# Kernel optimization log

Hardware: AMD Instinct MI355X
Metric: run time of the kernel (lower is better)

The kernel has to match this reference:

```python
import jax, jax.numpy as jnp
import numpy as np

EMBED_DIM = 1024
NUM_HEADS = 16
HEAD_DIM = EMBED_DIM // NUM_HEADS


def setup_inputs() -> dict:
    key = jax.random.key(0)
    ks = jax.random.split(key, 5)
    B, S, E = 2, 2048, EMBED_DIM
    # xavier-uniform-ish scale for square linear weights
    lim = float(np.sqrt(6.0 / (E + E)))
    x = jax.random.normal(ks[0], (B, S, E), dtype=jnp.float32)
    Wq = jax.random.uniform(ks[1], (E, E), jnp.float32, -lim, lim)
    Wk = jax.random.uniform(ks[2], (E, E), jnp.float32, -lim, lim)
    Wv = jax.random.uniform(ks[3], (E, E), jnp.float32, -lim, lim)
    Wo = jax.random.uniform(ks[4], (E, E), jnp.float32, -lim, lim)
    z = jnp.zeros((E,), jnp.float32)
    return {"x": x, "Wq": Wq, "bq": z, "Wk": Wk, "bk": z,
            "Wv": Wv, "bv": z, "Wo": Wo, "bo": z}


def reference(x, Wq, bq, Wk, bk, Wv, bv, Wo, bo):
    B, S, E = x.shape
    H, Dh = NUM_HEADS, HEAD_DIM
    # Linear projections (torch Linear: y = x @ W.T + b)
    q = (x @ Wq.T + bq).reshape(B, S, H, Dh).transpose(0, 2, 1, 3)  # [B,H,S,Dh]
    k = (x @ Wk.T + bk).reshape(B, S, H, Dh).transpose(0, 2, 1, 3)
    v = (x @ Wv.T + bv).reshape(B, S, H, Dh).transpose(0, 2, 1, 3)
    # NOTE: module scales by 1/head_dim (not 1/sqrt(head_dim)) — faithful.
    logits = jnp.einsum('bhqd,bhkd->bhqk', q, k) / Dh  # [B,H,S,S]
    attn = jax.nn.softmax(logits, axis=-1)
    vals = jnp.einsum('bhqk,bhkd->bhqd', attn, v)      # [B,H,S,Dh]
    vals = vals.transpose(0, 2, 1, 3).reshape(B, S, E)
    out = vals @ Wo.T + bo
    return out
```

## Files before the change

kernel.cpp:

```cpp
#include <hip/hip_runtime.h>
#include <hip/hip_bf16.h>

#define EDIM 1024
#define NH   16
#define DH   64
#define BB   2
#define SS   2048
#define MM   (BB*SS)

typedef unsigned short u16;
typedef unsigned int   u32;
typedef __attribute__((ext_vector_type(4)))  float f32x4;
typedef __attribute__((ext_vector_type(16))) float f32x16;
typedef __attribute__((ext_vector_type(8)))  short s16x8;

__device__ __forceinline__ u16 f2bf(float x) {
    __hip_bfloat16 b = __float2bfloat16(x);
    return *(u16*)&b;
}
__device__ __forceinline__ u32 cvtpk(float lo, float hi_) {
    u32 r;
    asm("v_cvt_pk_bf16_f32 %0, %1, %2" : "=v"(r) : "v"(lo), "v"(hi_));
    return r;
}
__device__ __forceinline__ void swap32(u32& a, u32& b) {
    asm("v_permlane32_swap_b32 %0, %1" : "+v"(a), "+v"(b));
}

__device__ __forceinline__ void gload16(const void* g, void* l) {
    __builtin_amdgcn_global_load_lds(
        (const __attribute__((address_space(1))) unsigned int*)g,
        (__attribute__((address_space(3))) unsigned int*)l, 16, 0, 0);
}

__global__ __launch_bounds__(256) void convert_all(const float* __restrict__ x,
                                                   const float* __restrict__ Wq,
                                                   const float* __restrict__ Wk,
                                                   const float* __restrict__ Wv,
                                                   const float* __restrict__ Wo,
                                                   u16* __restrict__ xh,
                                                   u16* __restrict__ wqkv,
                                                   u16* __restrict__ woh)
{
    const int i = blockIdx.x * 256 + threadIdx.x;
    const float* src; ushort4* dst; int off;
    if (i < 1048576)      { src = x;  dst = (ushort4*)xh;   off = i; }
    else if (i < 1310720) { src = Wq; dst = (ushort4*)wqkv; off = i - 1048576; }
    else if (i < 1572864) { src = Wk; dst = (ushort4*)wqkv; off = i - 1310720 + 262144; }
    else if (i < 1835008) { src = Wv; dst = (ushort4*)wqkv; off = i - 1572864 + 524288; }
    else                  { src = Wo; dst = (ushort4*)woh;  off = i - 1835008; }
    const int so = (i < 1048576) ? i
                 : (i < 1310720) ? (i - 1048576)
                 : (i < 1572864) ? (i - 1310720)
                 : (i < 1835008) ? (i - 1572864) : (i - 1835008);
    const float4 v = ((const float4*)src)[so];
    ushort4 h;
    h.x = f2bf(v.x); h.y = f2bf(v.y); h.z = f2bf(v.z); h.w = f2bf(v.w);
    dst[off] = h;
}

__global__ __launch_bounds__(256) void gemm_qkv(const u16* __restrict__ A,
                                                const u16* __restrict__ B,
                                                const float* __restrict__ bq,
                                                const float* __restrict__ bk,
                                                const float* __restrict__ bv,
                                                u16* __restrict__ qb,
                                                u16* __restrict__ kb,
                                                u16* __restrict__ vT)
{
    __shared__ __align__(16) u16 As[2][128][64];
    __shared__ __align__(16) u16 Bs[2][128][64];

    const int tid  = threadIdx.x;
    const int lane = tid & 63, wid = tid >> 6;
    const int wm = wid >> 1, wn = wid & 1;
    const int swz = (blockIdx.x & 7) * 96 + (blockIdx.x >> 3);
    const int m0 = (swz & 31) * 128;
    const int n0 = (swz >> 5) * 128;

    const char* Abase = (const char*)(A + (size_t)m0 * 1024);
    const char* Bbase = (const char*)(B + (size_t)n0 * 1024);

    f32x4 acc[4][4];
    #pragma unroll
    for (int i = 0; i < 4; ++i)
        #pragma unroll
        for (int j = 0; j < 4; ++j) acc[i][j] = f32x4{0.f, 0.f, 0.f, 0.f};

    auto stage = [&](int buf, int k0) {
        #pragma unroll
        for (int i = 0; i < 4; ++i) {
            const int flat = i * 256 + tid;
            const int row = flat >> 3, u = flat & 7;
            const size_t so = (size_t)row * 2048 + (size_t)k0 * 2 + ((u ^ (row & 7)) << 4);
            gload16(Abase + so, (char*)As + buf * 16384 + (i * 256 + wid * 64) * 16);
        }
        #pragma unroll
        for (int i = 0; i < 4; ++i) {
            const int flat = i * 256 + tid;
            const int row = flat >> 3, u = flat & 7;
            const size_t so = (size_t)row * 2048 + (size_t)k0 * 2 + ((u ^ (row & 7)) << 4);
            gload16(Bbase + so, (char*)Bs + buf * 16384 + (i * 256 + wid * 64) * 16);
        }
    };
    auto compute = [&](int buf) {
        const char* Ab = (const char*)As + buf * 16384;
        const char* Bb = (const char*)Bs + buf * 16384;
        #pragma unroll
        for (int kk = 0; kk < 2; ++kk) {
            s16x8 af[4], bfr[4];
            #pragma unroll
            for (int i = 0; i < 4; ++i) {
                const int rowA = wm * 64 + i * 16 + (lane & 15);
                af[i] = *(const s16x8*)(Ab + rowA * 128 + (((kk * 4 + (lane >> 4)) ^ (rowA & 7)) << 4));
                const int rowB = wn * 64 + i * 16 + (lane & 15);
                bfr[i] = *(const s16x8*)(Bb + rowB * 128 + (((kk * 4 + (lane >> 4)) ^ (rowB & 7)) << 4));
            }
            #pragma unroll
            for (int i = 0; i < 4; ++i)
                #pragma unroll
                for (int j = 0; j < 4; ++j)
                    acc[i][j] = __builtin_amdgcn_mfma_f32_16x16x32_bf16(af[i], bfr[j], acc[i][j], 0, 0, 0);
        }
    };

    stage(0, 0);
    __syncthreads();
    #pragma unroll 1
    for (int t = 0; t < 15; ++t) {
        stage((t & 1) ^ 1, (t + 1) * 64);
        compute(t & 1);
        __syncthreads();
    }
    compute(1);

    if (n0 < 1024) {
        #pragma unroll
        for (int i = 0; i < 4; ++i) {
            const int mbase = m0 + wm * 64 + i * 16 + ((lane >> 4) * 4);
            #pragma unroll
            for (int j = 0; j < 4; ++j) {
                const int n = n0 + wn * 64 + j * 16 + (lane & 15);
                const float bias = bq[n];
                const int h_ = n >> 6, d_ = n & 63;
                #pragma unroll
                for (int r = 0; r < 4; ++r) {
                    const int m = mbase + r;
                    const int b_ = m >> 11, s_ = m & 2047;
                    qb[((size_t)(b_ * NH + h_) * SS + s_) * DH + d_] = f2bf(acc[i][j][r] + bias);
                }
            }
        }
    } else if (n0 < 2048) {
        #pragma unroll
        for (int i = 0; i < 4; ++i) {
            const int mbase = m0 + wm * 64 + i * 16 + ((lane >> 4) * 4);
            #pragma unroll
            for (int j = 0; j < 4; ++j) {
                const int n = n0 + wn * 64 + j * 16 + (lane & 15);
                const float bias = bk[n - 1024];
                const int h_ = (n >> 6) & 15, d_ = n & 63;
                #pragma unroll
                for (int r = 0; r < 4; ++r) {
                    const int m = mbase + r;
                    const int b_ = m >> 11, s_ = m & 2047;
                    kb[((size_t)(b_ * NH + h_) * SS + s_) * DH + d_] = f2bf(acc[i][j][r] + bias);
                }
            }
        }
    } else {
        #pragma unroll
        for (int i = 0; i < 4; ++i) {
            const int mbase = m0 + wm * 64 + i * 16 + ((lane >> 4) * 4);
            #pragma unroll
            for (int j = 0; j < 4; ++j) {
                const int n = n0 + wn * 64 + j * 16 + (lane & 15);
                const float bias = bv[n - 2048];
                const int hd = n - 2048;
                #pragma unroll
                for (int r = 0; r < 4; ++r) {
                    const int m = mbase + r;
                    const int b_ = m >> 11, s_ = m & 2047;
                    vT[((size_t)(b_ * EDIM) + hd) * SS + s_] = f2bf(acc[i][j][r] + bias);
                }
            }
        }
    }
}

__global__ __launch_bounds__(256) void gemm_out(const u16* __restrict__ A,
                                                const u16* __restrict__ B,
                                                const float* __restrict__ bo,
                                                float* __restrict__ out)
{
    __shared__ __align__(16) u16 As[2][64][64];
    __shared__ __align__(16) u16 Bs[2][128][64];

    const int tid  = threadIdx.x;
    const int lane = tid & 63, wid = tid >> 6;
    const int wm = wid >> 1, wn = wid & 1;
    const int swz = (blockIdx.x & 7) * 64 + (blockIdx.x >> 3);
    const int m0 = (swz & 63) * 64;
    const int n0 = (swz >> 6) * 128;

    const char* Abase = (const char*)(A + (size_t)m0 * 1024);
    const char* Bbase = (const char*)(B + (size_t)n0 * 1024);

    f32x4 acc[2][4];
    #pragma unroll
    for (int i = 0; i < 2; ++i)
        #pragma unroll
        for (int j = 0; j < 4; ++j) acc[i][j] = f32x4{0.f, 0.f, 0.f, 0.f};

    auto stage = [&](int buf, int k0) {
        #pragma unroll
        for (int i = 0; i < 2; ++i) {
            const int flat = i * 256 + tid;
            const int row = flat >> 3, u = flat & 7;
            const size_t so = (size_t)row * 2048 + (size_t)k0 * 2 + ((u ^ (row & 7)) << 4);
            gload16(Abase + so, (char*)As + buf * 8192 + (i * 256 + wid * 64) * 16);
        }
        #pragma unroll
        for (int i = 0; i < 4; ++i) {
            const int flat = i * 256 + tid;
            const int row = flat >> 3, u = flat & 7;
            const size_t so = (size_t)row * 2048 + (size_t)k0 * 2 + ((u ^ (row & 7)) << 4);
            gload16(Bbase + so, (char*)Bs + buf * 16384 + (i * 256 + wid * 64) * 16);
        }
    };
    auto compute = [&](int buf) {
        const char* Ab = (const char*)As + buf * 8192;
        const char* Bb = (const char*)Bs + buf * 16384;
        #pragma unroll
        for (int kk = 0; kk < 2; ++kk) {
            s16x8 af[2], bfr[4];
            #pragma unroll
            for (int i = 0; i < 2; ++i) {
                const int rowA = wm * 32 + i * 16 + (lane & 15);
                af[i] = *(const s16x8*)(Ab + rowA * 128 + (((kk * 4 + (lane >> 4)) ^ (rowA & 7)) << 4));
            }
            #pragma unroll
            for (int j = 0; j < 4; ++j) {
                const int rowB = wn * 64 + j * 16 + (lane & 15);
                bfr[j] = *(const s16x8*)(Bb + rowB * 128 + (((kk * 4 + (lane >> 4)) ^ (rowB & 7)) << 4));
            }
            #pragma unroll
            for (int i = 0; i < 2; ++i)
                #pragma unroll
                for (int j = 0; j < 4; ++j)
                    acc[i][j] = __builtin_amdgcn_mfma_f32_16x16x32_bf16(af[i], bfr[j], acc[i][j], 0, 0, 0);
        }
    };

    stage(0, 0);
    __syncthreads();
    #pragma unroll 1
    for (int t = 0; t < 15; ++t) {
        stage((t & 1) ^ 1, (t + 1) * 64);
        compute(t & 1);
        __syncthreads();
    }
    compute(1);

    #pragma unroll
    for (int i = 0; i < 2; ++i) {
        const int mbase = m0 + wm * 32 + i * 16 + ((lane >> 4) * 4);
        #pragma unroll
        for (int j = 0; j < 4; ++j) {
            const int n = n0 + wn * 64 + j * 16 + (lane & 15);
            #pragma unroll
            for (int r = 0; r < 4; ++r)
                out[(size_t)(mbase + r) * EDIM + n] = acc[i][j][r] + bo[n];
        }
    }
}

__global__ __launch_bounds__(256) void attn_mfma(const u16* __restrict__ q,
                                                 const u16* __restrict__ k,
                                                 const u16* __restrict__ vT,
                                                 u16* __restrict__ valsh)
{
    __shared__ __align__(16) u16 kt[2][128][64];
    __shared__ __align__(16) u16 vt[2][64][128];

    const int tid = threadIdx.x, lane = tid & 63, wid = tid >> 6;
    const int lq = lane & 31, hi = lane >> 5;
    const int swz = (blockIdx.x & 7) * 64 + (blockIdx.x >> 3);
    const int bh = swz >> 4, qt = swz & 15;
    const int b = bh >> 4, h = bh & 15;

    const u16* qg = q + ((size_t)bh * SS + qt * 128 + wid * 32 + lq) * DH + hi * 8;
    s16x8 qf[4];
    #pragma unroll
    for (int ks = 0; ks < 4; ++ks) qf[ks] = *(const s16x8*)(qg + ks * 16);

    f32x16 acc_o[2];
    #pragma unroll
    for (int db = 0; db < 2; ++db)
        #pragma unroll
        for (int r = 0; r < 16; ++r) acc_o[db][r] = 0.f;
    float rs = 0.f;

    const char* kbh = (const char*)(k + (size_t)bh * SS * DH);
    const char* vbh = (const char*)(vT + ((size_t)b * EDIM + h * DH) * SS);

    auto stage = [&](int buf, int c0) {
        #pragma unroll
        for (int i = 0; i < 4; ++i) {
            const int flat = i * 256 + tid;
            const int row = flat >> 3, u = flat & 7;
            gload16(kbh + (size_t)(c0 + row) * 128 + ((u ^ (row & 7)) << 4),
                    (char*)kt + buf * 16384 + (i * 256 + wid * 64) * 16);
        }
        #pragma unroll
        for (int i = 0; i < 4; ++i) {
            const int flat = i * 256 + tid;
            const int row = flat >> 4, u = flat & 15;
            gload16(vbh + (size_t)row * (SS * 2) + (size_t)c0 * 2 + ((u ^ (row & 15)) << 4),
                    (char*)vt + buf * 16384 + (i * 256 + wid * 64) * 16);
        }
    };

    stage(0, 0);
    __syncthreads();

    int buf = 0;
    #pragma unroll 1
    for (int c = 0; c < 16; ++c) {
        if (c < 15) stage(buf ^ 1, (c + 1) * 128);
        const char* ktb = (const char*)kt + buf * 16384;
        const char* vtb = (const char*)vt + buf * 16384;

        #pragma unroll
        for (int kb = 0; kb < 4; ++kb) {
            f32x16 sc;
            #pragma unroll
            for (int r = 0; r < 16; ++r) sc[r] = 0.f;
            const int krow = kb * 32 + lq;
            __builtin_amdgcn_s_setprio(1);
            #pragma unroll
            for (int ks = 0; ks < 4; ++ks) {
                const int u = (ks * 2 + hi) ^ (krow & 7);
                const s16x8 kf = *(const s16x8*)(ktb + krow * 128 + u * 16);
                sc = __builtin_amdgcn_mfma_f32_32x32x16_bf16(kf, qf[ks], sc, 0, 0, 0);
            }
            __builtin_amdgcn_s_setprio(0);

            #pragma unroll
            for (int r = 0; r < 16; ++r) {
                sc[r] = __builtin_amdgcn_exp2f(sc[r] * 0.0225421209f);
                rs += sc[r];
            }

            u32 w0 = cvtpk(sc[0],  sc[1]),  w1 = cvtpk(sc[2],  sc[3]);
            u32 w2 = cvtpk(sc[4],  sc[5]),  w3 = cvtpk(sc[6],  sc[7]);
            u32 w4 = cvtpk(sc[8],  sc[9]),  w5 = cvtpk(sc[10], sc[11]);
            u32 w6 = cvtpk(sc[12], sc[13]), w7 = cvtpk(sc[14], sc[15]);
            swap32(w0, w2);
            swap32(w1, w3);
            swap32(w4, w6);
            swap32(w5, w7);
            union { u32 w[4]; s16x8 v; } pa0, pa1;
            pa0.w[0] = w0; pa0.w[1] = w1; pa0.w[2] = w2; pa0.w[3] = w3;
            pa1.w[0] = w4; pa1.w[1] = w5; pa1.w[2] = w6; pa1.w[3] = w7;

            __builtin_amdgcn_s_setprio(1);
            #pragma unroll
            for (int t = 0; t < 2; ++t) {
                const s16x8 pat = t ? pa1.v : pa0.v;
                const int kst = kb * 2 + t;
                #pragma unroll
                for (int db = 0; db < 2; ++db) {
                    const int vrow = db * 32 + lq;
                    const int u = (kst * 2 + hi) ^ (vrow & 15);
                    const s16x8 vf = *(const s16x8*)(vtb + vrow * 256 + u * 16);
                    acc_o[db] = __builtin_amdgcn_mfma_f32_32x32x16_bf16(pat, vf, acc_o[db], 0, 0, 0);
                }
            }
            __builtin_amdgcn_s_setprio(0);
        }
        __syncthreads();
        buf ^= 1;
    }

    const float rsf = rs + __shfl_xor(rs, 32, 64);
    const float inv = 1.f / rsf;
    float iv[16];
    #pragma unroll
    for (int r = 0; r < 16; ++r)
        iv[r] = __shfl(inv, (r & 3) + 8 * (r >> 2) + 4 * hi, 64);

    #pragma unroll
    for (int db = 0; db < 2; ++db)
        #pragma unroll
        for (int r = 0; r < 16; ++r) {
            const int srow = qt * 128 + wid * 32 + (r & 3) + 8 * (r >> 2) + 4 * hi;
            const int col  = h * 64 + db * 32 + lq;
            valsh[(size_t)(b * SS + srow) * EDIM + col] = f2bf(acc_o[db][r] * iv[r]);
        }
}

extern "C" void kernel_launch(void* const* d_in, const int* in_sizes, int n_in,
                              void* d_out, int out_size, void* d_ws, size_t ws_size,
                              hipStream_t stream)
{
    const float* x  = (const float*)d_in[0];
    const float* Wq = (const float*)d_in[1];
    const float* bq = (const float*)d_in[2];
    const float* Wk = (const float*)d_in[3];
    const float* bk = (const float*)d_in[4];
    const float* Wv = (const float*)d_in[5];
    const float* bv = (const float*)d_in[6];
    const float* Wo = (const float*)d_in[7];
    const float* bo = (const float*)d_in[8];
    float* out = (float*)d_out;

    u16* W = (u16*)d_ws;
    const size_t M1 = 1024 * 1024;
    u16* xh    = W;
    u16* wqkv  = W + 4  * M1;
    u16* woh   = W + 7  * M1;
    u16* qbuf  = W + 8  * M1;
    u16* kbuf  = W + 12 * M1;
    u16* vbufT = W + 16 * M1;
    u16* valsh = W + 20 * M1;

    convert_all<<<dim3(8192), 256, 0, stream>>>(x, Wq, Wk, Wv, Wo, xh, wqkv, woh);

    gemm_qkv<<<dim3(768), 256, 0, stream>>>(xh, wqkv, bq, bk, bv, qbuf, kbuf, vbufT);

    attn_mfma<<<dim3(BB * NH * (SS / 128)), 256, 0, stream>>>(qbuf, kbuf, vbufT, valsh);

    gemm_out<<<dim3(512), 256, 0, stream>>>(valsh, woh, bo, out);
}
```

Measured before the change: 210.6 us.

## Replace double-buffered LDS staging with single buffer in projection GEMMs

Both projection GEMMs (QKV and output) drop the two-stage LDS ping-pong and use a single LDS buffer: each k-step loads a tile, syncs, computes, then syncs again. The per-thread global offsets are also precomputed once outside the loop. This halves LDS use, which may let more blocks share a CU, but it gives up overlap between global-to-LDS loads and MFMA compute and adds a barrier per iteration.

```diff
diff --git a/kernel.cpp b/kernel.cpp
--- a/kernel.cpp
+++ b/kernel.cpp
@@ -68,8 +68,8 @@
                                                 u16* __restrict__ kb,
                                                 u16* __restrict__ vT)
 {
-    __shared__ __align__(16) u16 As[2][128][64];
-    __shared__ __align__(16) u16 Bs[2][128][64];
+    __shared__ __align__(16) u16 As[128][64];
+    __shared__ __align__(16) u16 Bs[128][64];
 
     const int tid  = threadIdx.x;
     const int lane = tid & 63, wid = tid >> 6;
@@ -78,6 +78,14 @@
     const int m0 = (swz & 31) * 128;
     const int n0 = (swz >> 5) * 128;
 
+    size_t aoff[4], boff[4];
+    #pragma unroll
+    for (int i = 0; i < 4; ++i) {
+        const int flat = i * 256 + tid;
+        const int row = flat >> 3, u = flat & 7;
+        const size_t o = (size_t)row * 2048 + ((u ^ (row & 7)) << 4);
+        aoff[i] = o; boff[i] = o;
+    }
     const char* Abase = (const char*)(A + (size_t)m0 * 1024);
     const char* Bbase = (const char*)(B + (size_t)n0 * 1024);
 
@@ -87,34 +95,26 @@
         #pragma unroll
         for (int j = 0; j < 4; ++j) acc[i][j] = f32x4{0.f, 0.f, 0.f, 0.f};
 
-    auto stage = [&](int buf, int k0) {
-        #pragma unroll
-        for (int i = 0; i < 4; ++i) {
-            const int flat = i * 256 + tid;
-            const int row = flat >> 3, u = flat & 7;
-            const size_t so = (size_t)row * 2048 + (size_t)k0 * 2 + ((u ^ (row & 7)) << 4);
-            gload16(Abase + so, (char*)As + buf * 16384 + (i * 256 + wid * 64) * 16);
-        }
-        #pragma unroll
-        for (int i = 0; i < 4; ++i) {
-            const int flat = i * 256 + tid;
-            const int row = flat >> 3, u = flat & 7;
-            const size_t so = (size_t)row * 2048 + (size_t)k0 * 2 + ((u ^ (row & 7)) << 4);
-            gload16(Bbase + so, (char*)Bs + buf * 16384 + (i * 256 + wid * 64) * 16);
-        }
-    };
-    auto compute = [&](int buf) {
-        const char* Ab = (const char*)As + buf * 16384;
-        const char* Bb = (const char*)Bs + buf * 16384;
+    #pragma unroll 1
+    for (int t = 0; t < 16; ++t) {
+        const size_t kb_ = (size_t)t * 128;
+        #pragma unroll
+        for (int i = 0; i < 4; ++i)
+            gload16(Abase + aoff[i] + kb_, (char*)As + (i * 256 + wid * 64) * 16);
+        #pragma unroll
+        for (int i = 0; i < 4; ++i)
+            gload16(Bbase + boff[i] + kb_, (char*)Bs + (i * 256 + wid * 64) * 16);
+        __syncthreads();
+
         #pragma unroll
         for (int kk = 0; kk < 2; ++kk) {
             s16x8 af[4], bfr[4];
             #pragma unroll
             for (int i = 0; i < 4; ++i) {
                 const int rowA = wm * 64 + i * 16 + (lane & 15);
-                af[i] = *(const s16x8*)(Ab + rowA * 128 + (((kk * 4 + (lane >> 4)) ^ (rowA & 7)) << 4));
+                af[i] = *(const s16x8*)((const char*)As + rowA * 128 + (((kk * 4 + (lane >> 4)) ^ (rowA & 7)) << 4));
                 const int rowB = wn * 64 + i * 16 + (lane & 15);
-                bfr[i] = *(const s16x8*)(Bb + rowB * 128 + (((kk * 4 + (lane >> 4)) ^ (rowB & 7)) << 4));
+                bfr[i] = *(const s16x8*)((const char*)Bs + rowB * 128 + (((kk * 4 + (lane >> 4)) ^ (rowB & 7)) << 4));
             }
             #pragma unroll
             for (int i = 0; i < 4; ++i)
@@ -122,17 +122,8 @@
                 for (int j = 0; j < 4; ++j)
                     acc[i][j] = __builtin_amdgcn_mfma_f32_16x16x32_bf16(af[i], bfr[j], acc[i][j], 0, 0, 0);
         }
-    };
-
-    stage(0, 0);
-    __syncthreads();
-    #pragma unroll 1
-    for (int t = 0; t < 15; ++t) {
-        stage((t & 1) ^ 1, (t + 1) * 64);
-        compute(t & 1);
         __syncthreads();
     }
-    compute(1);
 
     if (n0 < 1024) {
         #pragma unroll
@@ -193,8 +184,8 @@
                                                 const float* __restrict__ bo,
                                                 float* __restrict__ out)
 {
-    __shared__ __align__(16) u16 As[2][64][64];
-    __shared__ __align__(16) u16 Bs[2][128][64];
+    __shared__ __align__(16) u16 As[64][64];
+    __shared__ __align__(16) u16 Bs[128][64];
 
     const int tid  = threadIdx.x;
     const int lane = tid & 63, wid = tid >> 6;
@@ -203,6 +194,19 @@
     const int m0 = (swz & 63) * 64;
     const int n0 = (swz >> 6) * 128;
 
+    size_t aoff[2], boff[4];
+    #pragma unroll
+    for (int i = 0; i < 2; ++i) {
+        const int flat = i * 256 + tid;
+        const int row = flat >> 3, u = flat & 7;
+        aoff[i] = (size_t)row * 2048 + ((u ^ (row & 7)) << 4);
+    }
+    #pragma unroll
+    for (int i = 0; i < 4; ++i) {
+        const int flat = i * 256 + tid;
+        const int row = flat >> 3, u = flat & 7;
+        boff[i] = (size_t)row * 2048 + ((u ^ (row & 7)) << 4);
+    }
     const char* Abase = (const char*)(A + (size_t)m0 * 1024);
     const char* Bbase = (const char*)(B + (size_t)n0 * 1024);
 
@@ -212,37 +216,29 @@
         #pragma unroll
         for (int j = 0; j < 4; ++j) acc[i][j] = f32x4{0.f, 0.f, 0.f, 0.f};
 
-    auto stage = [&](int buf, int k0) {
-        #pragma unroll
-        for (int i = 0; i < 2; ++i) {
-            const int flat = i * 256 + tid;
-            const int row = flat >> 3, u = flat & 7;
-            const size_t so = (size_t)row * 2048 + (size_t)k0 * 2 + ((u ^ (row & 7)) << 4);
-            gload16(Abase + so, (char*)As + buf * 8192 + (i * 256 + wid * 64) * 16);
-        }
-        #pragma unroll
-        for (int i = 0; i < 4; ++i) {
-            const int flat = i * 256 + tid;
-            const int row = flat >> 3, u = flat & 7;
-            const size_t so = (size_t)row * 2048 + (size_t)k0 * 2 + ((u ^ (row & 7)) << 4);
-            gload16(Bbase + so, (char*)Bs + buf * 16384 + (i * 256 + wid * 64) * 16);
-        }
-    };
-    auto compute = [&](int buf) {
-        const char* Ab = (const char*)As + buf * 8192;
-        const char* Bb = (const char*)Bs + buf * 16384;
+    #pragma unroll 1
+    for (int t = 0; t < 16; ++t) {
+        const size_t kb_ = (size_t)t * 128;
+        #pragma unroll
+        for (int i = 0; i < 2; ++i)
+            gload16(Abase + aoff[i] + kb_, (char*)As + (i * 256 + wid * 64) * 16);
+        #pragma unroll
+        for (int i = 0; i < 4; ++i)
+            gload16(Bbase + boff[i] + kb_, (char*)Bs + (i * 256 + wid * 64) * 16);
+        __syncthreads();
+
         #pragma unroll
         for (int kk = 0; kk < 2; ++kk) {
             s16x8 af[2], bfr[4];
             #pragma unroll
             for (int i = 0; i < 2; ++i) {
                 const int rowA = wm * 32 + i * 16 + (lane & 15);
-                af[i] = *(const s16x8*)(Ab + rowA * 128 + (((kk * 4 + (lane >> 4)) ^ (rowA & 7)) << 4));
+                af[i] = *(const s16x8*)((const char*)As + rowA * 128 + (((kk * 4 + (lane >> 4)) ^ (rowA & 7)) << 4));
             }
             #pragma unroll
             for (int j = 0; j < 4; ++j) {
                 const int rowB = wn * 64 + j * 16 + (lane & 15);
-                bfr[j] = *(const s16x8*)(Bb + rowB * 128 + (((kk * 4 + (lane >> 4)) ^ (rowB & 7)) << 4));
+                bfr[j] = *(const s16x8*)((const char*)Bs + rowB * 128 + (((kk * 4 + (lane >> 4)) ^ (rowB & 7)) << 4));
             }
             #pragma unroll
             for (int i = 0; i < 2; ++i)
@@ -250,17 +246,8 @@
                 for (int j = 0; j < 4; ++j)
                     acc[i][j] = __builtin_amdgcn_mfma_f32_16x16x32_bf16(af[i], bfr[j], acc[i][j], 0, 0, 0);
         }
-    };
-
-    stage(0, 0);
-    __syncthreads();
-    #pragma unroll 1
-    for (int t = 0; t < 15; ++t) {
-        stage((t & 1) ^ 1, (t + 1) * 64);
-        compute(t & 1);
         __syncthreads();
     }
-    compute(1);
 
     #pragma unroll
     for (int i = 0; i < 2; ++i) {
```

Measured after the change: 204.2 us. 3.1% less time.
